# Kernel tuning notes

Measured on AMD Instinct MI355X. Metric: run time of the kernel, lower is better.

## Reference

```python
import jax, jax.numpy as jnp
import numpy as np
import math

DIM = 768
EMB = 768          # dim * num_heads (num_heads=1)
NBLOCKS = 4
M = EMB // 2       # kernel_ratio = 0.5 -> 384 random features
EPS = 1e-8


def monarch_linear(x, w1, w2, b):
    """Monarch (blockdiag butterfly) linear: x [..., n] -> [..., out].
    w1: (k, q, p) with n = k*p ; w2: (l, s, r) with k*q = l*r ; out = l*s."""
    lead = x.shape[:-1]
    k, q, p = w1.shape
    l, s, r = w2.shape
    xf = x.reshape(-1, k, p)                              # (B, k, p)
    o1 = jnp.einsum('bkp,kqp->bkq', xf, w1)               # (B, k, q)
    o1 = o1.transpose(0, 2, 1).reshape(-1, l, r)          # permute then (B, l, r)
    o2 = jnp.einsum('blr,lsr->bls', o1, w2)               # (B, l, s)
    out = o2.transpose(0, 2, 1).reshape(*lead, s * l)     # (B, s, l) flattened
    return out + b


def prm_exp(x, w):
    """FAVOR+ positive random features. x: [b,t,d], w: [m,d]."""
    xd = 0.5 * jnp.sum(x * x, axis=-1, keepdims=True)     # [b,t,1]
    wtx = jnp.einsum('btd,md->btm', x, w)                 # [b,t,m]
    return jnp.exp(wtx - xd) / math.sqrt(M)


def _monarch_params(rng, n_in, n_out, nblocks):
    in_blk = n_in // nblocks
    out_blk = n_out // nblocks
    if n_in < n_out:
        w1 = rng.standard_normal((nblocks, in_blk, in_blk)).astype(np.float32)
        w2 = rng.standard_normal((nblocks, out_blk, in_blk)).astype(np.float32)
    else:
        w1 = rng.standard_normal((nblocks, out_blk, in_blk)).astype(np.float32)
        w2 = rng.standard_normal((nblocks, out_blk, out_blk)).astype(np.float32)
    scale = 1.0 / math.sqrt(n_in)
    b = rng.standard_normal((n_out,)).astype(np.float32) * scale
    return w1 * scale, w2 * scale, b


def setup_inputs() -> dict:
    key = jax.random.key(0)
    x = jax.random.normal(key, (8, 4096, DIM), dtype=jnp.float32)
    rng = np.random.default_rng(0)
    kqv_w1, kqv_w2, kqv_b = _monarch_params(rng, DIM, 3 * EMB, NBLOCKS)
    proj_w1, proj_w2, proj_b = _monarch_params(rng, EMB, EMB, NBLOCKS)
    # orthogonal random-feature matrix, rows orthonormal, scaled by sqrt(m)
    a = rng.standard_normal((EMB, M)).astype(np.float64)
    qmat, _ = np.linalg.qr(a)                             # (EMB, M), cols orthonormal
    w = (qmat.T * math.sqrt(M)).astype(np.float32)        # (M, EMB)
    return {
        'x': x,
        'kqv_w1': jnp.asarray(kqv_w1), 'kqv_w2': jnp.asarray(kqv_w2), 'kqv_b': jnp.asarray(kqv_b),
        'proj_w1': jnp.asarray(proj_w1), 'proj_w2': jnp.asarray(proj_w2), 'proj_b': jnp.asarray(proj_b),
        'w': jnp.asarray(w),
    }


def reference(x, kqv_w1, kqv_w2, kqv_b, proj_w1, proj_w2, proj_b, w):
    kqv = monarch_linear(x, kqv_w1, kqv_w2, kqv_b)        # [b,t,3*EMB]
    k, q, v = jnp.split(kqv, 3, axis=-1)                  # order k,q,v as in torch.split
    kp = prm_exp(k, w)                                    # [b,t,m]
    qp = prm_exp(q, w)                                    # [b,t,m]
    D = jnp.einsum('btm,bm->bt', qp, kp.sum(axis=1))[:, :, None]   # [b,t,1]
    kptv = jnp.einsum('btn,btm->bnm', v, kp)              # [b,EMB,m]
    y = jnp.einsum('btm,bnm->btn', qp, kptv) / (D + EPS)  # [b,t,EMB]
    return monarch_linear(y, proj_w1, proj_w2, proj_b)
```

## Files before the change

kernel.cpp:

```cpp
#include <hip/hip_runtime.h>


#define NTOK   32768
#define RSQRTM 0.05103103630798288f

typedef _Float16 f16;
typedef f16   f16x8 __attribute__((ext_vector_type(8)));
typedef f16   f16x4 __attribute__((ext_vector_type(4)));
typedef short s16x8 __attribute__((ext_vector_type(8)));
typedef float f32x4 __attribute__((ext_vector_type(4)));

typedef const void __attribute__((address_space(1))) gv_t;
typedef void       __attribute__((address_space(3))) lv_t;
#define GLL16(g, l) __builtin_amdgcn_global_load_lds((gv_t*)(g), (lv_t*)(l), 16, 0, 0)

__device__ __forceinline__ float b2f(unsigned short u){
  union{unsigned int i; float f;} v; v.i = ((unsigned int)u)<<16; return v.f;
}
__device__ __forceinline__ unsigned short f2b(float f){
  union{float f; unsigned int i;} v; v.f = f;
  unsigned int x = v.i;
  x += 0x7fffu + ((x>>16)&1u);
  return (unsigned short)(x>>16);
}

template<typename T> struct MfmaOp;
template<> struct MfmaOp<f16> {
  typedef f16x8 frag;
  static __device__ __forceinline__ f32x4 run(frag a, frag b, f32x4 c){
    return __builtin_amdgcn_mfma_f32_16x16x32_f16(a, b, c, 0, 0, 0);
  }
};
template<> struct MfmaOp<short> {
  typedef s16x8 frag;
  static __device__ __forceinline__ f32x4 run(frag a, frag b, f32x4 c){
    return __builtin_amdgcn_mfma_f32_16x16x32_bf16(a, b, c, 0, 0, 0);
  }
};

__global__ void cvt16(const float4* __restrict__ src, f16* __restrict__ dst, int n4){
  const int i = blockIdx.x*256 + threadIdx.x;
  if (i >= n4) return;
  const float4 v = src[i];
  f16x4 h; h[0]=(f16)v.x; h[1]=(f16)v.y; h[2]=(f16)v.z; h[3]=(f16)v.w;
  *reinterpret_cast<f16x4*>(dst + 4*(long)i) = h;
}
__global__ void build_wkqvT(const float* __restrict__ w1, const float* __restrict__ w2,
                            f16* __restrict__ Wt){
  const int idx = blockIdx.x*256 + threadIdx.x;
  const int j = idx / 768, i = idx % 768;
  const int k = i / 192, p = i % 192;
  const int s = j >> 2,  l = j & 3;
  float acc = 0.f;
  #pragma unroll 4
  for(int u=0; u<48; ++u)
    acc += w1[(k*192 + l*48+u)*192 + p] * w2[(l*576+s)*192 + 4*u+k];
  Wt[idx] = (f16)acc;
}
__global__ void build_wprojT(const float* __restrict__ w1, const float* __restrict__ w2,
                             unsigned short* __restrict__ Wt){
  const int idx = blockIdx.x*256 + threadIdx.x;
  const int j = idx / 768, i = idx % 768;
  const int k = i / 192, p = i % 192;
  const int s = j >> 2,  l = j & 3;
  float acc = 0.f;
  #pragma unroll 4
  for(int u=0; u<48; ++u)
    acc += w1[(k*192 + l*48+u)*192 + p] * w2[(l*192+s)*192 + 4*u+k];
  Wt[idx] = f2b(acc);
}
__global__ void reduce_kptv_t(const float* __restrict__ p32, unsigned short* __restrict__ o){
  __shared__ float t[64][65];
  const int b = blockIdx.z, n0 = blockIdx.x*64, m0 = blockIdx.y*64;
  const int tx = threadIdx.x & 63, ty = threadIdx.x >> 6;
  const float* base = p32 + (long)b*4*294912;
  #pragma unroll 4
  for (int r = 0; r < 16; ++r){
    const int n = n0 + ty*16 + r;
    const int idx = n*384 + m0 + tx;
    t[tx][ty*16+r] = base[idx] + base[294912+idx] + base[2*294912+idx] + base[3*294912+idx];
  }
  __syncthreads();
  unsigned short* ob = o + (long)b*294912;
  #pragma unroll 4
  for (int r = 0; r < 16; ++r){
    const int m = m0 + ty*16 + r;
    ob[(long)m*768 + n0 + tx] = f2b(t[ty*16+r][tx]);
  }
}

template<typename T, int BM, int BN, int EPI, int SPLIT>
__global__ __launch_bounds__(256)
void mgemm(const T* __restrict__ A, int lda, long aB,
           const T* __restrict__ Bt, int ldb, long bB,
           int K, void* __restrict__ out, int ldo, long outB,
           void* __restrict__ out2,
           const float* __restrict__ aux, long auxB,
           float* __restrict__ aux2){
  constexpr int MT = BM/32, NT = BN/32;
  constexpr int IA = BM/32, IB = BN/32;
  __shared__ T As[BM*64];
  __shared__ T Bs[BN*64];
  typedef typename MfmaOp<T>::frag frag_t;

  const int tid = threadIdx.x, lane = tid & 63, w = tid >> 6;
  const int wm = w >> 1, wn = w & 1;
  const int ln = lane & 15, q = lane >> 4;
  const int bz = blockIdx.z;
  const int batch = bz / SPLIT;
  const int kstart = (bz % SPLIT) * K;
  const long m0 = (long)blockIdx.y * BM;
  const int  n0 = blockIdx.x * BN;
  const T* Ab = A  + (long)batch*aB;
  const T* Bb = Bt + (long)batch*bB;

  f32x4 acc[MT][NT];
  const f32x4 zero = {0.f, 0.f, 0.f, 0.f};
  #pragma unroll
  for(int i=0;i<MT;i++)
    #pragma unroll
    for(int j=0;j<NT;j++) acc[i][j] = zero;

  for (int k0 = kstart; k0 < kstart + K; k0 += 64){
    __syncthreads();
    #pragma unroll
    for (int i = 0; i < IA; ++i){
      const int e = (w*IA + i)*64 + lane;
      const int m = e >> 3, j = (e & 7) ^ (m & 7);
      GLL16(Ab + (m0 + m)*lda + k0 + j*8, As + (size_t)(w*IA + i)*512);
    }
    #pragma unroll
    for (int i = 0; i < IB; ++i){
      const int e = (w*IB + i)*64 + lane;
      const int n = e >> 3, j = (e & 7) ^ (n & 7);
      GLL16(Bb + (long)(n0 + n)*ldb + k0 + j*8, Bs + (size_t)(w*IB + i)*512);
    }
    __syncthreads();

    #pragma unroll
    for (int kk = 0; kk < 2; ++kk){
      frag_t a[MT], b[NT];
      #pragma unroll
      for (int mt=0; mt<MT; ++mt){
        const int r = wm*MT*16 + mt*16 + ln;
        a[mt] = *reinterpret_cast<const frag_t*>(&As[(r*8 + ((kk*4+q) ^ (r&7)))*8]);
      }
      #pragma unroll
      for (int nt=0; nt<NT; ++nt){
        const int r = wn*NT*16 + nt*16 + ln;
        b[nt] = *reinterpret_cast<const frag_t*>(&Bs[(r*8 + ((kk*4+q) ^ (r&7)))*8]);
      }
      #pragma unroll
      for (int mt=0; mt<MT; ++mt)
        #pragma unroll
        for (int nt=0; nt<NT; ++nt)
          acc[mt][nt] = MfmaOp<T>::run(a[mt], b[nt], acc[mt][nt]);
    }
  }

  if constexpr(EPI==1){
    const int b = (int)(m0 >> 12);
    float cs[NT];
    #pragma unroll
    for(int nt=0;nt<NT;nt++) cs[nt]=0.f;
    #pragma unroll
    for (int mt=0; mt<MT; ++mt){
      const long mbase = m0 + wm*MT*16 + mt*16 + q*4;
      float xv[4];
      #pragma unroll
      for(int r=0;r<4;r++) xv[r] = aux[mbase + r];
      #pragma unroll
      for (int nt=0; nt<NT; ++nt){
        const int n = n0 + wn*NT*16 + nt*16 + ln;
        const f32x4 c = acc[mt][nt];
        ushort4 v;
        v.x = f2b(__expf(c[0]-xv[0])*RSQRTM);
        v.y = f2b(__expf(c[1]-xv[1])*RSQRTM);
        v.z = f2b(__expf(c[2]-xv[2])*RSQRTM);
        v.w = f2b(__expf(c[3]-xv[3])*RSQRTM);
        *reinterpret_cast<ushort4*>(&((unsigned short*)out)[(long)n*ldo + mbase]) = v;
        cs[nt] += b2f(v.x)+b2f(v.y)+b2f(v.z)+b2f(v.w);
      }
    }
    #pragma unroll
    for (int nt=0; nt<NT; ++nt){
      cs[nt] += __shfl_xor(cs[nt], 16);
      cs[nt] += __shfl_xor(cs[nt], 32);
      if (lane < 16)
        atomicAdd(&aux2[b*384 + n0 + wn*NT*16 + nt*16 + lane], cs[nt]);
    }
    return;
  }

  #pragma unroll
  for (int mt=0; mt<MT; ++mt){
    const long mbase = m0 + wm*MT*16 + mt*16 + q*4;
    if constexpr(EPI==0){
      const int nw = n0 + wn*NT*16;
      const int part = nw / 768;
      float p[4] = {0.f,0.f,0.f,0.f};
      #pragma unroll
      for (int nt=0; nt<NT; ++nt){
        const int n = nw + nt*16 + ln;
        const f32x4 c = acc[mt][nt];
        const float bv = aux[n];
        if (part < 2){
          f16* KQ = (f16*)out;
          #pragma unroll
          for(int r=0;r<4;r++){
            const f16 h = (f16)(c[r] + bv);
            KQ[(mbase+r)*1536 + n] = h;
            const float hf = (float)h;
            p[r] += hf*hf;
          }
        } else {
          unsigned short* VT = (unsigned short*)out2;
          ushort4 v;
          v.x = f2b(c[0]+bv); v.y = f2b(c[1]+bv); v.z = f2b(c[2]+bv); v.w = f2b(c[3]+bv);
          *reinterpret_cast<ushort4*>(&VT[(long)(n-1536)*32768 + mbase]) = v;
        }
      }
      if (part < 2){
        #pragma unroll
        for(int r=0;r<4;r++){
          #pragma unroll
          for(int mask=1; mask<16; mask<<=1) p[r] += __shfl_xor(p[r], mask);
        }
        if (ln == 0){
          #pragma unroll
          for(int r=0;r<4;r++)
            atomicAdd(&aux2[part*NTOK + mbase + r], 0.5f*p[r]);
        }
      }
    } else if constexpr(EPI==2){
      const int b = (int)(m0 >> 12);
      float xv[4], dp[4] = {0.f,0.f,0.f,0.f};
      #pragma unroll
      for(int r=0;r<4;r++) xv[r] = aux[mbase + r];
      #pragma unroll
      for (int nt=0; nt<NT; ++nt){
        const int n = n0 + wn*NT*16 + nt*16 + ln;
        const f32x4 c = acc[mt][nt];
        const float ksn = aux2[b*384 + n];
        #pragma unroll
        for(int r=0;r<4;r++){
          const unsigned short h = f2b(__expf(c[r]-xv[r])*RSQRTM);
          ((unsigned short*)out)[(mbase+r)*ldo + n] = h;
          dp[r] += b2f(h)*ksn;
        }
      }
      #pragma unroll
      for(int r=0;r<4;r++){
        #pragma unroll
        for(int mask=1; mask<16; mask<<=1) dp[r] += __shfl_xor(dp[r], mask);
      }
      if (ln == 0){
        #pragma unroll
        for(int r=0;r<4;r++)
          atomicAdd(&((float*)out2)[mbase + r], dp[r]);
      }
    } else if constexpr(EPI==3){
      float* o = (float*)out + (long)bz*outB;
      #pragma unroll
      for (int nt=0; nt<NT; ++nt){
        const int n = n0 + wn*NT*16 + nt*16 + ln;
        const f32x4 c = acc[mt][nt];
        #pragma unroll
        for(int r=0;r<4;r++) o[(mbase+r)*ldo + n] = c[r];
      }
    } else if constexpr(EPI==6){
      unsigned short* o = (unsigned short*)out + (long)bz*outB;
      #pragma unroll
      for (int nt=0; nt<NT; ++nt){
        const int n = n0 + wn*NT*16 + nt*16 + ln;
        const f32x4 c = acc[mt][nt];
        #pragma unroll
        for(int r=0;r<4;r++) o[(mbase+r)*ldo + n] = f2b(c[r]);
      }
    } else if constexpr(EPI==7){
      float* o = (float*)out + (long)bz*outB;
      float xv[4];
      #pragma unroll
      for(int r=0;r<4;r++) xv[r] = 1.f/(aux[bz*auxB + mbase + r] + 1e-8f);
      #pragma unroll
      for (int nt=0; nt<NT; ++nt){
        const int n = n0 + wn*NT*16 + nt*16 + ln;
        const f32x4 c = acc[mt][nt];
        const float bv = aux2[n];
        #pragma unroll
        for(int r=0;r<4;r++) o[(mbase+r)*ldo + n] = c[r]*xv[r] + bv;
      }
    }
  }
}

extern "C" void kernel_launch(void* const* d_in, const int* in_sizes, int n_in,
                              void* d_out, int out_size, void* d_ws, size_t ws_size,
                              hipStream_t stream){
  (void)in_sizes; (void)n_in; (void)out_size;
  const float* x       = (const float*)d_in[0];
  const float* kqv_w1  = (const float*)d_in[1];
  const float* kqv_w2  = (const float*)d_in[2];
  const float* kqv_b   = (const float*)d_in[3];
  const float* proj_w1 = (const float*)d_in[4];
  const float* proj_w2 = (const float*)d_in[5];
  const float* proj_b  = (const float*)d_in[6];
  const float* w       = (const float*)d_in[7];
  char* ws = (char*)d_ws;

  const size_t o_WkqvT  = 0;
  const size_t o_WprojT = 3538944;
  const size_t o_w16    = 4718592;
  const size_t o_x16    = 5308416;
  const size_t o_KQ     = 55640064;
  const size_t o_VT     = 156303360;
  const size_t o_xd     = 206635008;
  const size_t o_ksum   = 206897152;
  const size_t o_Dv     = 206909440;
  const size_t o_kpT    = 207040512;
  const size_t o_qp     = 232206336;
  const size_t o_kptv32 = 257372160;
  const size_t o_kptvT  = 295120896;
  const size_t o_Z      = 299839488;
  const size_t TOTAL    = 304558080;
  if (ws_size < TOTAL) return;

  f16*            WkqvT  = (f16*)(ws + o_WkqvT);
  short*          WprojT = (short*)(ws + o_WprojT);
  f16*            w16    = (f16*)(ws + o_w16);
  f16*            x16    = (f16*)(ws + o_x16);
  f16*            KQ     = (f16*)(ws + o_KQ);
  short*          VT     = (short*)(ws + o_VT);
  float*          xd     = (float*)(ws + o_xd);
  float*          ksum   = (float*)(ws + o_ksum);
  float*          Dv     = (float*)(ws + o_Dv);
  short*          kpT    = (short*)(ws + o_kpT);
  short*          qp     = (short*)(ws + o_qp);
  float*          kptv32 = (float*)(ws + o_kptv32);
  unsigned short* kptvT  = (unsigned short*)(ws + o_kptvT);
  short*          Z      = (short*)(ws + o_Z);

  hipMemsetAsync(ws + o_xd, 0, 405504, stream);

  cvt16<<<24576, 256, 0, stream>>>((const float4*)x, x16, 6291456);
  cvt16<<<288,   256, 0, stream>>>((const float4*)w, w16, 73728);
  build_wkqvT <<<6912, 256, 0, stream>>>(kqv_w1, kqv_w2, WkqvT);
  build_wprojT<<<2304, 256, 0, stream>>>(proj_w1, proj_w2, (unsigned short*)WprojT);

  mgemm<f16,128,128,0,1><<<dim3(18,256,1), 256, 0, stream>>>(
      x16, 768, 0L, WkqvT, 768, 0L, 768, KQ, 1536, 0L, VT, kqv_b, 0L, xd);

  mgemm<f16,128,128,1,1><<<dim3(3,256,1), 256, 0, stream>>>(
      KQ, 1536, 0L, w16, 768, 0L, 768, kpT, 32768, 0L, nullptr, xd, 0L, ksum);

  mgemm<f16,128,128,2,1><<<dim3(3,256,1), 256, 0, stream>>>(
      KQ + 768, 1536, 0L, w16, 768, 0L, 768, qp, 384, 0L, Dv, xd + NTOK, 0L, ksum);

  mgemm<short,128,128,3,4><<<dim3(3,6,32), 256, 0, stream>>>(
      VT, 32768, 4096L, kpT, 32768, 4096L, 1024, kptv32, 384, 294912L,
      nullptr, nullptr, 0L, nullptr);

  reduce_kptv_t<<<dim3(12,6,8), 256, 0, stream>>>(kptv32, kptvT);

  mgemm<short,128,128,6,1><<<dim3(3,6,8), 256, 0, stream>>>(
      WprojT, 768, 0L, (short*)kptvT, 768, 294912L, 768, Z, 384, 294912L,
      nullptr, nullptr, 0L, nullptr);

  mgemm<short,128,128,7,1><<<dim3(6,32,8), 256, 0, stream>>>(
      qp, 384, 1572864L, Z, 384, 294912L, 384, d_out, 768, 3145728L,
      nullptr, Dv, 4096L, (float*)proj_b);
}
```

Baseline: 613.9 us.

## Fold random-feature matrix into K/Q projection weights to skip KQ buffer

Precomputes the product of the random-feature matrix with the K and Q slices of the fused monarch weight, plus the bias term, so the kp and qp GEMMs read x16 directly instead of a materialized KQ activation. The first GEMM no longer writes the 100MB fp16 KQ buffer and keeps it only to compute the squared norms. This removes a large write and reread of KQ in exchange for a small weight-prep GEMM and extra fp16 rounding of the combined weights. The first GEMM still does the full K/Q matmul just to get the norms, so its MFMA work is unchanged.

```diff
diff --git a/kernel.cpp b/kernel.cpp
--- a/kernel.cpp
+++ b/kernel.cpp
@@ -46,7 +46,7 @@
   *reinterpret_cast<f16x4*>(dst + 4*(long)i) = h;
 }
 __global__ void build_wkqvT(const float* __restrict__ w1, const float* __restrict__ w2,
-                            f16* __restrict__ Wt){
+                            f16* __restrict__ Wt, f16* __restrict__ Wn){
   const int idx = blockIdx.x*256 + threadIdx.x;
   const int j = idx / 768, i = idx % 768;
   const int k = i / 192, p = i % 192;
@@ -56,6 +56,7 @@
   for(int u=0; u<48; ++u)
     acc += w1[(k*192 + l*48+u)*192 + p] * w2[(l*576+s)*192 + 4*u+k];
   Wt[idx] = (f16)acc;
+  if (j < 1536) Wn[(long)i*1536 + j] = (f16)acc;
 }
 __global__ void build_wprojT(const float* __restrict__ w1, const float* __restrict__ w2,
                              unsigned short* __restrict__ Wt){
@@ -69,6 +70,17 @@
     acc += w1[(k*192 + l*48+u)*192 + p] * w2[(l*192+s)*192 + 4*u+k];
   Wt[idx] = f2b(acc);
 }
+__global__ void build_bkw(const float* __restrict__ b, const f16* __restrict__ w16,
+                          float* __restrict__ bkw){
+  const int idx = blockIdx.x*256 + threadIdx.x;
+  if (idx >= 768) return;
+  const int part = idx / 384, m = idx % 384;
+  const float* bp = b + part*768;
+  const f16*  wp = w16 + (long)m*768;
+  float acc = 0.f;
+  for(int j=0; j<768; ++j) acc += bp[j]*(float)wp[j];
+  bkw[idx] = acc;
+}
 __global__ void reduce_kptv_t(const float* __restrict__ p32, unsigned short* __restrict__ o){
   __shared__ float t[64][65];
   const int b = blockIdx.z, n0 = blockIdx.x*64, m0 = blockIdx.y*64;
@@ -96,7 +108,8 @@
            int K, void* __restrict__ out, int ldo, long outB,
            void* __restrict__ out2,
            const float* __restrict__ aux, long auxB,
-           float* __restrict__ aux2){
+           float* __restrict__ aux2,
+           const float* __restrict__ bias){
   constexpr int MT = BM/32, NT = BN/32;
   constexpr int IA = BM/32, IB = BN/32;
   __shared__ T As[BM*64];
@@ -173,11 +186,12 @@
       for (int nt=0; nt<NT; ++nt){
         const int n = n0 + wn*NT*16 + nt*16 + ln;
         const f32x4 c = acc[mt][nt];
+        const float bn = bias[n];
         ushort4 v;
-        v.x = f2b(__expf(c[0]-xv[0])*RSQRTM);
-        v.y = f2b(__expf(c[1]-xv[1])*RSQRTM);
-        v.z = f2b(__expf(c[2]-xv[2])*RSQRTM);
-        v.w = f2b(__expf(c[3]-xv[3])*RSQRTM);
+        v.x = f2b(__expf(c[0]+bn-xv[0])*RSQRTM);
+        v.y = f2b(__expf(c[1]+bn-xv[1])*RSQRTM);
+        v.z = f2b(__expf(c[2]+bn-xv[2])*RSQRTM);
+        v.w = f2b(__expf(c[3]+bn-xv[3])*RSQRTM);
         *reinterpret_cast<ushort4*>(&((unsigned short*)out)[(long)n*ldo + mbase]) = v;
         cs[nt] += b2f(v.x)+b2f(v.y)+b2f(v.z)+b2f(v.w);
       }
@@ -205,11 +219,9 @@
         const f32x4 c = acc[mt][nt];
         const float bv = aux[n];
         if (part < 2){
-          f16* KQ = (f16*)out;
           #pragma unroll
           for(int r=0;r<4;r++){
             const f16 h = (f16)(c[r] + bv);
-            KQ[(mbase+r)*1536 + n] = h;
             const float hf = (float)h;
             p[r] += hf*hf;
           }
@@ -241,10 +253,11 @@
       for (int nt=0; nt<NT; ++nt){
         const int n = n0 + wn*NT*16 + nt*16 + ln;
         const f32x4 c = acc[mt][nt];
+        const float bn = bias[n];
         const float ksn = aux2[b*384 + n];
         #pragma unroll
         for(int r=0;r<4;r++){
-          const unsigned short h = f2b(__expf(c[r]-xv[r])*RSQRTM);
+          const unsigned short h = f2b(__expf(c[r]+bn-xv[r])*RSQRTM);
           ((unsigned short*)out)[(mbase+r)*ldo + n] = h;
           dp[r] += b2f(h)*ksn;
         }
@@ -289,6 +302,15 @@
         const float bv = aux2[n];
         #pragma unroll
         for(int r=0;r<4;r++) o[(mbase+r)*ldo + n] = c[r]*xv[r] + bv;
+      }
+    } else if constexpr(EPI==8){
+      f16* o = (f16*)out + (long)bz*outB;
+      #pragma unroll
+      for (int nt=0; nt<NT; ++nt){
+        const int n = n0 + wn*NT*16 + nt*16 + ln;
+        const f32x4 c = acc[mt][nt];
+        #pragma unroll
+        for(int r=0;r<4;r++) o[(mbase+r)*ldo + n] = (f16)c[r];
       }
     }
   }
@@ -309,27 +331,31 @@
   char* ws = (char*)d_ws;
 
   const size_t o_WkqvT  = 0;
-  const size_t o_WprojT = 3538944;
-  const size_t o_w16    = 4718592;
-  const size_t o_x16    = 5308416;
-  const size_t o_KQ     = 55640064;
-  const size_t o_VT     = 156303360;
-  const size_t o_xd     = 206635008;
-  const size_t o_ksum   = 206897152;
-  const size_t o_Dv     = 206909440;
-  const size_t o_kpT    = 207040512;
-  const size_t o_qp     = 232206336;
-  const size_t o_kptv32 = 257372160;
-  const size_t o_kptvT  = 295120896;
-  const size_t o_Z      = 299839488;
-  const size_t TOTAL    = 304558080;
+  const size_t o_WkqvN  = 3538944;
+  const size_t o_WprojT = 5898240;
+  const size_t o_w16    = 7077888;
+  const size_t o_Wkw    = 7667712;
+  const size_t o_bkw    = 8847360;
+  const size_t o_x16    = 8850432;
+  const size_t o_VT     = 59182080;
+  const size_t o_xd     = 109513728;
+  const size_t o_ksum   = 109775872;
+  const size_t o_Dv     = 109788160;
+  const size_t o_kpT    = 109919232;
+  const size_t o_qp     = 135085056;
+  const size_t o_kptv32 = 160250880;
+  const size_t o_kptvT  = 197999616;
+  const size_t o_Z      = 202718208;
+  const size_t TOTAL    = 207436800;
   if (ws_size < TOTAL) return;
 
   f16*            WkqvT  = (f16*)(ws + o_WkqvT);
+  f16*            WkqvN  = (f16*)(ws + o_WkqvN);
   short*          WprojT = (short*)(ws + o_WprojT);
   f16*            w16    = (f16*)(ws + o_w16);
+  f16*            Wkw    = (f16*)(ws + o_Wkw);
+  float*          bkw    = (float*)(ws + o_bkw);
   f16*            x16    = (f16*)(ws + o_x16);
-  f16*            KQ     = (f16*)(ws + o_KQ);
   short*          VT     = (short*)(ws + o_VT);
   float*          xd     = (float*)(ws + o_xd);
   float*          ksum   = (float*)(ws + o_ksum);
@@ -344,29 +370,35 @@
 
   cvt16<<<24576, 256, 0, stream>>>((const float4*)x, x16, 6291456);
   cvt16<<<288,   256, 0, stream>>>((const float4*)w, w16, 73728);
-  build_wkqvT <<<6912, 256, 0, stream>>>(kqv_w1, kqv_w2, WkqvT);
+  build_wkqvT <<<6912, 256, 0, stream>>>(kqv_w1, kqv_w2, WkqvT, WkqvN);
   build_wprojT<<<2304, 256, 0, stream>>>(proj_w1, proj_w2, (unsigned short*)WprojT);
+  build_bkw   <<<3,    256, 0, stream>>>(kqv_b, w16, bkw);
+
+  mgemm<f16,128,128,8,1><<<dim3(6,3,2), 256, 0, stream>>>(
+      w16, 768, 0L, WkqvN, 1536, 768L, 768, Wkw, 768, 294912L,
+      nullptr, nullptr, 0L, nullptr, nullptr);
 
   mgemm<f16,128,128,0,1><<<dim3(18,256,1), 256, 0, stream>>>(
-      x16, 768, 0L, WkqvT, 768, 0L, 768, KQ, 1536, 0L, VT, kqv_b, 0L, xd);
+      x16, 768, 0L, WkqvT, 768, 0L, 768, nullptr, 0, 0L, VT, kqv_b, 0L, xd, nullptr);
 
   mgemm<f16,128,128,1,1><<<dim3(3,256,1), 256, 0, stream>>>(
-      KQ, 1536, 0L, w16, 768, 0L, 768, kpT, 32768, 0L, nullptr, xd, 0L, ksum);
+      x16, 768, 0L, Wkw, 768, 0L, 768, kpT, 32768, 0L, nullptr, xd, 0L, ksum, bkw);
 
   mgemm<f16,128,128,2,1><<<dim3(3,256,1), 256, 0, stream>>>(
-      KQ + 768, 1536, 0L, w16, 768, 0L, 768, qp, 384, 0L, Dv, xd + NTOK, 0L, ksum);
+      x16, 768, 0L, Wkw + 294912, 768, 0L, 768, qp, 384, 0L, Dv,
+      xd + NTOK, 0L, ksum, bkw + 384);
 
   mgemm<short,128,128,3,4><<<dim3(3,6,32), 256, 0, stream>>>(
       VT, 32768, 4096L, kpT, 32768, 4096L, 1024, kptv32, 384, 294912L,
-      nullptr, nullptr, 0L, nullptr);
+      nullptr, nullptr, 0L, nullptr, nullptr);
 
   reduce_kptv_t<<<dim3(12,6,8), 256, 0, stream>>>(kptv32, kptvT);
 
   mgemm<short,128,128,6,1><<<dim3(3,6,8), 256, 0, stream>>>(
       WprojT, 768, 0L, (short*)kptvT, 768, 294912L, 768, Z, 384, 294912L,
-      nullptr, nullptr, 0L, nullptr);
+      nullptr, nullptr, 0L, nullptr, nullptr);
 
   mgemm<short,128,128,7,1><<<dim3(6,32,8), 256, 0, stream>>>(
       qp, 384, 1572864L, Z, 384, 294912L, 384, d_out, 768, 3145728L,
-      nullptr, Dv, 4096L, (float*)proj_b);
-}
+      nullptr, Dv, 4096L, (float*)proj_b, nullptr);
+}
```

Measured after the change: 640.9 us. 1.04x slower.

## Split KQV GEMM per output part and transpose kptv via swapped operands

Applied to the files above, without the earlier changes.

The fused KQV GEMM is split into three launches (K, Q, V) so each launch has a uniform epilogue, with an n-offset passed through outB. The V part gets its own epilogue variant. The kptv split-K GEMM swaps its A/B operands so it writes the transposed layout directly, and the shared-memory transpose reduction becomes a plain elementwise sum with bf16 conversion. This removes epilogue branch divergence and the LDS transpose, at the cost of two extra kernel launches.

```diff
diff --git a/kernel.cpp b/kernel.cpp
--- a/kernel.cpp
+++ b/kernel.cpp
@@ -69,24 +69,11 @@
     acc += w1[(k*192 + l*48+u)*192 + p] * w2[(l*192+s)*192 + 4*u+k];
   Wt[idx] = f2b(acc);
 }
-__global__ void reduce_kptv_t(const float* __restrict__ p32, unsigned short* __restrict__ o){
-  __shared__ float t[64][65];
-  const int b = blockIdx.z, n0 = blockIdx.x*64, m0 = blockIdx.y*64;
-  const int tx = threadIdx.x & 63, ty = threadIdx.x >> 6;
-  const float* base = p32 + (long)b*4*294912;
-  #pragma unroll 4
-  for (int r = 0; r < 16; ++r){
-    const int n = n0 + ty*16 + r;
-    const int idx = n*384 + m0 + tx;
-    t[tx][ty*16+r] = base[idx] + base[294912+idx] + base[2*294912+idx] + base[3*294912+idx];
-  }
-  __syncthreads();
-  unsigned short* ob = o + (long)b*294912;
-  #pragma unroll 4
-  for (int r = 0; r < 16; ++r){
-    const int m = m0 + ty*16 + r;
-    ob[(long)m*768 + n0 + tx] = f2b(t[ty*16+r][tx]);
-  }
+__global__ void reduce_kptv(const float* __restrict__ p32, unsigned short* __restrict__ o){
+  const int idx = blockIdx.x*256 + threadIdx.x;
+  const int b = idx / 294912, i = idx % 294912;
+  const float* base = p32 + (long)b*4*294912 + i;
+  o[idx] = f2b(base[0] + base[294912] + base[2*294912] + base[3*294912]);
 }
 
 template<typename T, int BM, int BN, int EPI, int SPLIT>
@@ -110,7 +97,7 @@
   const int batch = bz / SPLIT;
   const int kstart = (bz % SPLIT) * K;
   const long m0 = (long)blockIdx.y * BM;
-  const int  n0 = blockIdx.x * BN;
+  const int  n0 = blockIdx.x * BN + ((EPI==0 || EPI==9) ? (int)outB : 0);
   const T* Ab = A  + (long)batch*aB;
   const T* Bb = Bt + (long)batch*bB;
 
@@ -204,33 +191,35 @@
         const int n = nw + nt*16 + ln;
         const f32x4 c = acc[mt][nt];
         const float bv = aux[n];
-        if (part < 2){
-          f16* KQ = (f16*)out;
-          #pragma unroll
-          for(int r=0;r<4;r++){
-            const f16 h = (f16)(c[r] + bv);
-            KQ[(mbase+r)*1536 + n] = h;
-            const float hf = (float)h;
-            p[r] += hf*hf;
-          }
-        } else {
-          unsigned short* VT = (unsigned short*)out2;
-          ushort4 v;
-          v.x = f2b(c[0]+bv); v.y = f2b(c[1]+bv); v.z = f2b(c[2]+bv); v.w = f2b(c[3]+bv);
-          *reinterpret_cast<ushort4*>(&VT[(long)(n-1536)*32768 + mbase]) = v;
+        f16* KQ = (f16*)out;
+        #pragma unroll
+        for(int r=0;r<4;r++){
+          const f16 h = (f16)(c[r] + bv);
+          KQ[(mbase+r)*1536 + n] = h;
+          const float hf = (float)h;
+          p[r] += hf*hf;
         }
       }
-      if (part < 2){
-        #pragma unroll
-        for(int r=0;r<4;r++){
-          #pragma unroll
-          for(int mask=1; mask<16; mask<<=1) p[r] += __shfl_xor(p[r], mask);
-        }
-        if (ln == 0){
-          #pragma unroll
-          for(int r=0;r<4;r++)
-            atomicAdd(&aux2[part*NTOK + mbase + r], 0.5f*p[r]);
-        }
+      #pragma unroll
+      for(int r=0;r<4;r++){
+        #pragma unroll
+        for(int mask=1; mask<16; mask<<=1) p[r] += __shfl_xor(p[r], mask);
+      }
+      if (ln == 0){
+        #pragma unroll
+        for(int r=0;r<4;r++)
+          atomicAdd(&aux2[part*NTOK + mbase + r], 0.5f*p[r]);
+      }
+    } else if constexpr(EPI==9){
+      #pragma unroll
+      for (int nt=0; nt<NT; ++nt){
+        const int n = n0 + wn*NT*16 + nt*16 + ln;
+        const f32x4 c = acc[mt][nt];
+        const float bv = aux[n];
+        unsigned short* VT = (unsigned short*)out2;
+        ushort4 v;
+        v.x = f2b(c[0]+bv); v.y = f2b(c[1]+bv); v.z = f2b(c[2]+bv); v.w = f2b(c[3]+bv);
+        *reinterpret_cast<ushort4*>(&VT[(long)(n-1536)*32768 + mbase]) = v;
       }
     } else if constexpr(EPI==2){
       const int b = (int)(m0 >> 12);
@@ -347,8 +336,12 @@
   build_wkqvT <<<6912, 256, 0, stream>>>(kqv_w1, kqv_w2, WkqvT);
   build_wprojT<<<2304, 256, 0, stream>>>(proj_w1, proj_w2, (unsigned short*)WprojT);
 
-  mgemm<f16,128,128,0,1><<<dim3(18,256,1), 256, 0, stream>>>(
-      x16, 768, 0L, WkqvT, 768, 0L, 768, KQ, 1536, 0L, VT, kqv_b, 0L, xd);
+  mgemm<f16,128,128,0,1><<<dim3(6,256,1), 256, 0, stream>>>(
+      x16, 768, 0L, WkqvT, 768, 0L, 768, KQ, 1536, 0L, nullptr, kqv_b, 0L, xd);
+  mgemm<f16,128,128,0,1><<<dim3(6,256,1), 256, 0, stream>>>(
+      x16, 768, 0L, WkqvT, 768, 0L, 768, KQ, 1536, 768L, nullptr, kqv_b, 0L, xd);
+  mgemm<f16,128,128,9,1><<<dim3(6,256,1), 256, 0, stream>>>(
+      x16, 768, 0L, WkqvT, 768, 0L, 768, nullptr, 0, 1536L, VT, kqv_b, 0L, nullptr);
 
   mgemm<f16,128,128,1,1><<<dim3(3,256,1), 256, 0, stream>>>(
       KQ, 1536, 0L, w16, 768, 0L, 768, kpT, 32768, 0L, nullptr, xd, 0L, ksum);
@@ -356,11 +349,11 @@
   mgemm<f16,128,128,2,1><<<dim3(3,256,1), 256, 0, stream>>>(
       KQ + 768, 1536, 0L, w16, 768, 0L, 768, qp, 384, 0L, Dv, xd + NTOK, 0L, ksum);
 
-  mgemm<short,128,128,3,4><<<dim3(3,6,32), 256, 0, stream>>>(
-      VT, 32768, 4096L, kpT, 32768, 4096L, 1024, kptv32, 384, 294912L,
+  mgemm<short,128,128,3,4><<<dim3(6,3,32), 256, 0, stream>>>(
+      kpT, 32768, 4096L, VT, 32768, 4096L, 1024, kptv32, 768, 294912L,
       nullptr, nullptr, 0L, nullptr);
 
-  reduce_kptv_t<<<dim3(12,6,8), 256, 0, stream>>>(kptv32, kptvT);
+  reduce_kptv<<<9216, 256, 0, stream>>>(kptv32, kptvT);
 
   mgemm<short,128,128,6,1><<<dim3(3,6,8), 256, 0, stream>>>(
       WprojT, 768, 0L, (short*)kptvT, 768, 294912L, 768, Z, 384, 294912L,
```

New measurement: 648.8 us. 1.06x slower.
